# Kernel tuning notes

Hardware: AMD Instinct MI355X
Metric: run time of the kernel (lower is better)

## Reference

```python
import jax, jax.numpy as jnp
import numpy as np

B, N, D, H, HD, C = 2, 2048, 2048, 16, 128, 128  # batch, seq, embed, heads, head_dim, chunk
EPS = 1e-6


def setup_inputs() -> dict:
    key = jax.random.key(0)
    ks = jax.random.split(key, 9)
    s = 0.02
    x = jax.random.normal(ks[0], (B, N, D), jnp.float32)
    # per-head negative log decay (lambda = exp(log_decay) in (0,1))
    log_decay = -jax.random.uniform(ks[1], (H,), jnp.float32, minval=0.01, maxval=1.0)
    Wq = jax.random.normal(ks[2], (D, D), jnp.float32) * s
    Wk = jax.random.normal(ks[3], (D, D), jnp.float32) * s
    Wv = jax.random.normal(ks[4], (D, D), jnp.float32) * s
    Wo = jax.random.normal(ks[5], (D, D), jnp.float32) * s
    Wg1 = jax.random.normal(ks[6], (D, HD), jnp.float32) * s
    Wg2 = jax.random.normal(ks[7], (HD, D), jnp.float32) * s
    norm_w = jnp.ones((D,), jnp.float32)
    return dict(x=x, log_decay=log_decay, Wq=Wq, Wk=Wk, Wv=Wv, Wo=Wo,
                Wg1=Wg1, Wg2=Wg2, norm_w=norm_w)


def _lasd(q, k, v, ld):
    # causal linear attention with per-head scalar log-decay, chunked scan.
    # q,k,v: [B,N,H,HD]; ld: [H] (negative). Recurrence: S_t = exp(ld)*S_{t-1} + k_t v_t^T; o_t = q_t @ S_t
    nc = N // C
    to_chunks = lambda t: t.reshape(B, nc, C, H, HD).transpose(1, 0, 3, 2, 4)  # [nc,B,H,C,HD]
    qc, kc, vc = map(to_chunks, (q, k, v))
    i = jnp.arange(C, dtype=jnp.float32)
    diff = i[:, None] - i[None, :]                     # [C,C]
    Dm = jnp.exp(jnp.where(diff >= 0, ld[:, None, None] * diff, -jnp.inf))  # [H,C,C]
    dq = jnp.exp(ld[:, None] * (i + 1.0))              # [H,C] decay applied to q vs chunk-start state
    dk = jnp.exp(ld[:, None] * (C - 1.0 - i))          # [H,C] decay applied to k for state update
    dS = jnp.exp(ld * C)                               # [H]   chunk-level state decay

    def step(S, qkv):
        qb, kb, vb = qkv                               # [B,H,C,HD]
        attn = jnp.einsum('bhid,bhjd->bhij', qb, kb) * Dm
        o = jnp.einsum('bhij,bhje->bhie', attn, vb)
        o = o + jnp.einsum('bhid,bhde->bhie', qb * dq[None, :, :, None], S)
        S = S * dS[None, :, None, None] + jnp.einsum('bhjd,bhje->bhde', kb * dk[None, :, :, None], vb)
        return S, o

    S0 = jnp.zeros((B, H, HD, HD), jnp.float32)
    _, o = jax.lax.scan(step, S0, (qc, kc, vc))        # [nc,B,H,C,HD]
    return o.transpose(1, 0, 3, 2, 4).reshape(B, N, H, HD)


def reference(x, log_decay, Wq, Wk, Wv, Wo, Wg1, Wg2, norm_w):
    silu = jax.nn.silu
    q = silu(x @ Wq).reshape(B, N, H, HD)
    k = silu(x @ Wk).reshape(B, N, H, HD)
    v = silu(x @ Wv).reshape(B, N, H, HD)
    o = _lasd(q, k, v, log_decay).reshape(B, N, D)
    gate = jax.nn.sigmoid((x @ Wg1) @ Wg2)             # two stacked linears, no nonlinearity between
    o = o * gate
    o = o * jax.lax.rsqrt(jnp.mean(o * o, axis=-1, keepdims=True) + EPS) * norm_w  # rmsnorm
    return o @ Wo
```

## Files before the change

### kernel.cpp

```cpp
#include <hip/hip_runtime.h>
#include <hip/hip_bf16.h>
#include <cstdint>
#include <cstddef>

#define B_   2
#define N_   2048
#define D_   2048
#define H_   16
#define HD_  128
#define C_   128
#define NC_  16
#define M_   4096
#define QKVG_ 8192

typedef __attribute__((ext_vector_type(8))) short bf16x8;
typedef __attribute__((ext_vector_type(4))) float f32x4;
typedef __attribute__((ext_vector_type(16))) float f32x16;

__device__ __forceinline__ uint16_t f2bf(float f){
  __hip_bfloat16 h = __float2bfloat16(f);
  return *reinterpret_cast<uint16_t*>(&h);
}
__device__ __forceinline__ float bf2f(uint16_t u){
  union { uint32_t i; float f; } v; v.i = ((uint32_t)u) << 16; return v.f;
}

__device__ __forceinline__ void async16(const uint16_t* g, uint16_t* l){
  __builtin_amdgcn_global_load_lds(
      (const __attribute__((address_space(1))) void*)g,
      (__attribute__((address_space(3))) void*)l, 16, 0, 0);
}

__device__ __forceinline__ int swz(int row, int c){
  return row*128 + ((((c >> 3) ^ row) & 15) << 3) + (c & 7);
}

__global__ __launch_bounds__(256) void cast_kernel(
    const float* __restrict__ x, uint16_t* __restrict__ y)
{
  int i = (blockIdx.x*256 + threadIdx.x)*4;
  float4 f = *(const float4*)(x + i);
  ushort4 u;
  u.x = f2bf(f.x); u.y = f2bf(f.y); u.z = f2bf(f.z); u.w = f2bf(f.w);
  *(ushort4*)(y + i) = u;
}

__global__ __launch_bounds__(256)
void prep_weights(const float* __restrict__ Wq, const float* __restrict__ Wk,
                  const float* __restrict__ Wv, const float* __restrict__ Wo,
                  const float* __restrict__ Wg2, const float* __restrict__ Wg1,
                  uint16_t* __restrict__ WT, uint16_t* __restrict__ WoT,
                  uint16_t* __restrict__ Wg2T, uint16_t* __restrict__ Wg1b)
{
  const int z = blockIdx.z;
  const int tx = threadIdx.x & 31;
  const int ty = threadIdx.x >> 5;
  __shared__ uint16_t tile[32][33];

  if (z == 5){
    if (blockIdx.x >= 4) return;
    const int r0 = blockIdx.y*32, c0 = blockIdx.x*32;
    #pragma unroll
    for (int rr = 0; rr < 4; ++rr){
      int r = r0 + ty + rr*8;
      Wg1b[(size_t)r*HD_ + c0 + tx] = f2bf(Wg1[(size_t)r*HD_ + c0 + tx]);
    }
    return;
  }

  const float* src; uint16_t* dst; int R, Cc;
  if (z < 3)      { src = (z==0)?Wq:(z==1)?Wk:Wv; dst = WT + (size_t)z*D_*D_; R = D_; Cc = D_; }
  else if (z == 3){ src = Wo;  dst = WoT;  R = D_;  Cc = D_; }
  else            { if (blockIdx.y >= 4) return;
                    src = Wg2; dst = Wg2T; R = HD_; Cc = D_; }

  const int r0 = blockIdx.y*32, c0 = blockIdx.x*32;
  #pragma unroll
  for (int rr = 0; rr < 4; ++rr){
    int r = ty + rr*8;
    tile[r][tx] = f2bf(src[(size_t)(r0 + r)*Cc + c0 + tx]);
  }
  __syncthreads();
  #pragma unroll
  for (int rr = 0; rr < 4; ++rr){
    int r = ty + rr*8;
    dst[(size_t)(c0 + r)*R + r0 + tx] = tile[tx][r];
  }
}

template<int ACT, int OUTBF>
__global__ __launch_bounds__(256)
void gemm_bt2(const uint16_t* __restrict__ A, const uint16_t* __restrict__ Bt,
              void* __restrict__ Cout, int M, int Ncols, int K, int klen)
{
  __shared__ __align__(16) uint16_t As[128*64];
  __shared__ __align__(16) uint16_t Bs[128*64];
  const int t    = threadIdx.x;
  const int lane = t & 63, wave = t >> 6;
  const int wm = wave >> 1, wn = wave & 1;
  const int row0 = wm*64, col0 = wn*64;
  const int lm = lane & 31, lh = lane >> 5;

  const uint16_t* Ap = A  + (size_t)(blockIdx.y*128)*K;
  const uint16_t* Bp = Bt + (size_t)(blockIdx.x*128)*K;
  const int kbeg = blockIdx.z * klen;

  f32x16 acc[2][2];
  #pragma unroll
  for (int i = 0; i < 2; ++i)
    #pragma unroll
    for (int j = 0; j < 2; ++j)
      #pragma unroll
      for (int r = 0; r < 16; ++r) acc[i][j][r] = 0.f;

  const int srow = t >> 3;
  const int gch  = (t & 7) ^ (srow & 7);
  const size_t aoff0 = (size_t)srow*K + gch*8;

  for (int k0 = kbeg; k0 < kbeg + klen; k0 += 64){
    #pragma unroll
    for (int c = 0; c < 4; ++c){
      async16(Ap + (size_t)(c*32)*K + aoff0 + k0, As + c*2048 + t*8);
      async16(Bp + (size_t)(c*32)*K + aoff0 + k0, Bs + c*2048 + t*8);
    }
    __syncthreads();
    #pragma unroll
    for (int kh = 0; kh < 4; ++kh){
      bf16x8 af[2], bfr[2];
      const int ch = kh*2 + lh;
      #pragma unroll
      for (int i = 0; i < 2; ++i){
        int r = row0 + i*32 + lm;
        af[i] = *(const bf16x8*)(As + r*64 + ((ch ^ (r & 7)) << 3));
      }
      #pragma unroll
      for (int j = 0; j < 2; ++j){
        int r = col0 + j*32 + lm;
        bfr[j] = *(const bf16x8*)(Bs + r*64 + ((ch ^ (r & 7)) << 3));
      }
      #pragma unroll
      for (int i = 0; i < 2; ++i)
        #pragma unroll
        for (int j = 0; j < 2; ++j)
          acc[i][j] = __builtin_amdgcn_mfma_f32_32x32x16_bf16(af[i], bfr[j], acc[i][j], 0, 0, 0);
    }
    __syncthreads();
  }

  const int mode = (ACT == 3) ? ((blockIdx.x < 48) ? 1 : 2) : ACT;
  uint16_t* outb = (uint16_t*)Cout;
  float*    outf = (float*)Cout + (OUTBF ? 0 : (size_t)blockIdx.z*M*Ncols);
  #pragma unroll
  for (int i = 0; i < 2; ++i){
    #pragma unroll
    for (int j = 0; j < 2; ++j){
      #pragma unroll
      for (int r = 0; r < 16; ++r){
        int row = blockIdx.y*128 + row0 + i*32 + (r & 3) + 8*(r >> 2) + 4*lh;
        int col = blockIdx.x*128 + col0 + j*32 + lm;
        float v = acc[i][j][r];
        if (mode == 1)      v = v / (1.f + __expf(-v));
        else if (mode == 2) v = 1.f / (1.f + __expf(-v));
        size_t off = (size_t)row*Ncols + col;
        if (OUTBF) outb[off] = f2bf(v);
        else       outf[off] = v;
      }
    }
  }
}

__global__ __launch_bounds__(256)
void add_kernel(const float* __restrict__ p0, const float* __restrict__ p1,
                float* __restrict__ out)
{
  int i = (blockIdx.x*256 + threadIdx.x)*4;
  float4 a = *(const float4*)(p0 + i);
  float4 b = *(const float4*)(p1 + i);
  float4 o; o.x = a.x+b.x; o.y = a.y+b.y; o.z = a.z+b.z; o.w = a.w+b.w;
  *(float4*)(out + i) = o;
}

__global__ __launch_bounds__(256)
void chunk_state_kernel(const uint16_t* __restrict__ qkvg,
                        const float* __restrict__ log_decay, uint16_t* __restrict__ MsumT)
{
  __shared__ __align__(16) uint16_t vT[128*128];
  __shared__ __align__(16) uint16_t kT[128*128];
  const int h = blockIdx.x, b = blockIdx.y, ic = blockIdx.z;
  const int t    = threadIdx.x;
  const int lane = t & 63, wave = t >> 6;
  const int wm = wave >> 1, wn = wave & 1;
  const int e0 = wm*64, d0 = wn*64;
  const int lr = lane & 15, kq = lane >> 4;
  const float ld = log_decay[h];
  const size_t rowbase = (size_t)b*N_ + (size_t)ic*C_;
  const uint16_t* kb = qkvg + (size_t)D_;
  const uint16_t* vb = qkvg + (size_t)2*D_;

  #pragma unroll 4
  for (int it = 0; it < 64; ++it){
    int idx = t + it*256;
    int j = idx >> 7, e = idx & 127;
    uint16_t vv = vb[(rowbase + j)*QKVG_ + h*HD_ + e];
    float kf = bf2f(kb[(rowbase + j)*QKVG_ + h*HD_ + e]) * __expf(ld * (float)(C_ - 1 - j));
    vT[swz(e, j)] = vv;
    kT[swz(e, j)] = f2bf(kf);
  }
  __syncthreads();

  const f32x4 zero = {0.f, 0.f, 0.f, 0.f};
  f32x4 acc[4][4];
  #pragma unroll
  for (int i = 0; i < 4; ++i)
    #pragma unroll
    for (int j = 0; j < 4; ++j) acc[i][j] = zero;

  #pragma unroll
  for (int kt = 0; kt < 4; ++kt){
    bf16x8 af[4], bfr[4];
    #pragma unroll
    for (int i = 0; i < 4; ++i)
      af[i]  = *(const bf16x8*)(vT + swz(e0 + i*16 + lr, kt*32 + kq*8));
    #pragma unroll
    for (int j = 0; j < 4; ++j)
      bfr[j] = *(const bf16x8*)(kT + swz(d0 + j*16 + lr, kt*32 + kq*8));
    #pragma unroll
    for (int i = 0; i < 4; ++i)
      #pragma unroll
      for (int j = 0; j < 4; ++j)
        acc[i][j] = __builtin_amdgcn_mfma_f32_16x16x32_bf16(af[i], bfr[j], acc[i][j], 0, 0, 0);
  }

  uint16_t* Mout = MsumT + (((size_t)ic*B_ + b)*H_ + h)*(size_t)(HD_*HD_);
  #pragma unroll
  for (int i = 0; i < 4; ++i)
    #pragma unroll
    for (int j = 0; j < 4; ++j)
      #pragma unroll
      for (int r = 0; r < 4; ++r)
        Mout[(size_t)(e0 + i*16 + kq*4 + r)*HD_ + d0 + j*16 + lr] = f2bf(acc[i][j][r]);
}

__global__ __launch_bounds__(256)
void scan_kernel(const uint16_t* __restrict__ MsumT, const float* __restrict__ log_decay,
                 uint16_t* __restrict__ StT)
{
  const int h = blockIdx.x, b = blockIdx.y;
  const float ld = log_decay[h];
  const float dS = __expf(ld * (float)C_);
  const int base_e = blockIdx.z*2048;
  float cur[8];
  #pragma unroll
  for (int r = 0; r < 8; ++r) cur[r] = 0.f;
  for (int i = 0; i < NC_; ++i){
    const size_t base = (((size_t)i*B_ + b)*H_ + h)*(size_t)(HD_*HD_) + base_e;
    #pragma unroll
    for (int r = 0; r < 8; ++r){
      int idx = threadIdx.x + r*256;
      StT[base + idx] = f2bf(cur[r]);
      cur[r] = cur[r]*dS + bf2f(MsumT[base + idx]);
    }
  }
}

__global__ __launch_bounds__(256)
void attn_kernel(const uint16_t* __restrict__ qkvg, const uint16_t* __restrict__ StT,
                 const float* __restrict__ log_decay, float* __restrict__ o_attn)
{
  __shared__ __align__(16) uint16_t Ps[128*128];
  __shared__ __align__(16) uint16_t vT[128*128];
  const int h = blockIdx.x, b = blockIdx.y, ic = blockIdx.z;
  const int t    = threadIdx.x;
  const int lane = t & 63, wave = t >> 6;
  const int wm = wave >> 1, wn = wave & 1;
  const int row0 = wm*64, col0 = wn*64;
  const int lr = lane & 15, kq = lane >> 4;
  const float ld = log_decay[h];
  const size_t rowbase = (size_t)b*N_ + (size_t)ic*C_;
  const uint16_t* qb = qkvg;
  const uint16_t* kb = qkvg + (size_t)D_;
  const uint16_t* vb = qkvg + (size_t)2*D_;

  #pragma unroll 4
  for (int it = 0; it < 64; ++it){
    int idx = t + it*256;
    int j = idx >> 7, e = idx & 127;
    vT[swz(e, j)] = vb[(rowbase + j)*QKVG_ + h*HD_ + e];
  }

  const f32x4 zero = {0.f, 0.f, 0.f, 0.f};
  f32x4 acc[4][4];
  #pragma unroll
  for (int i = 0; i < 4; ++i)
    #pragma unroll
    for (int j = 0; j < 4; ++j) acc[i][j] = zero;

  #pragma unroll
  for (int kt = 0; kt < 4; ++kt){
    bf16x8 af[4], bfr[4];
    #pragma unroll
    for (int i = 0; i < 4; ++i)
      af[i]  = *(const bf16x8*)(qb + (rowbase + row0 + i*16 + lr)*QKVG_ + h*HD_ + kt*32 + kq*8);
    #pragma unroll
    for (int j = 0; j < 4; ++j)
      bfr[j] = *(const bf16x8*)(kb + (rowbase + col0 + j*16 + lr)*QKVG_ + h*HD_ + kt*32 + kq*8);
    #pragma unroll
    for (int i = 0; i < 4; ++i)
      #pragma unroll
      for (int j = 0; j < 4; ++j)
        acc[i][j] = __builtin_amdgcn_mfma_f32_16x16x32_bf16(af[i], bfr[j], acc[i][j], 0, 0, 0);
  }
  #pragma unroll
  for (int i = 0; i < 4; ++i)
    #pragma unroll
    for (int j = 0; j < 4; ++j)
      #pragma unroll
      for (int r = 0; r < 4; ++r){
        int row = row0 + i*16 + kq*4 + r;
        int col = col0 + j*16 + lr;
        int dlt = row - col;
        float f = (dlt >= 0) ? __expf(ld * (float)dlt) : 0.f;
        Ps[swz(row, col)] = f2bf(acc[i][j][r] * f);
      }

  #pragma unroll
  for (int i = 0; i < 4; ++i)
    #pragma unroll
    for (int j = 0; j < 4; ++j) acc[i][j] = zero;
  const uint16_t* Sb = StT + (((size_t)ic*B_ + b)*H_ + h)*(size_t)(HD_*HD_);
  #pragma unroll
  for (int kt = 0; kt < 4; ++kt){
    bf16x8 af[4], bfr[4];
    #pragma unroll
    for (int i = 0; i < 4; ++i)
      af[i]  = *(const bf16x8*)(qb + (rowbase + row0 + i*16 + lr)*QKVG_ + h*HD_ + kt*32 + kq*8);
    #pragma unroll
    for (int j = 0; j < 4; ++j)
      bfr[j] = *(const bf16x8*)(Sb + (size_t)(col0 + j*16 + lr)*HD_ + kt*32 + kq*8);
    #pragma unroll
    for (int i = 0; i < 4; ++i)
      #pragma unroll
      for (int j = 0; j < 4; ++j)
        acc[i][j] = __builtin_amdgcn_mfma_f32_16x16x32_bf16(af[i], bfr[j], acc[i][j], 0, 0, 0);
  }
  #pragma unroll
  for (int i = 0; i < 4; ++i)
    #pragma unroll
    for (int r = 0; r < 4; ++r){
      float dqv = __expf(ld * (float)(row0 + i*16 + kq*4 + r + 1));
      #pragma unroll
      for (int j = 0; j < 4; ++j) acc[i][j][r] *= dqv;
    }

  __syncthreads();

  #pragma unroll
  for (int kt = 0; kt < 4; ++kt){
    bf16x8 af[4], bfr[4];
    #pragma unroll
    for (int i = 0; i < 4; ++i)
      af[i]  = *(const bf16x8*)(Ps + swz(row0 + i*16 + lr, kt*32 + kq*8));
    #pragma unroll
    for (int j = 0; j < 4; ++j)
      bfr[j] = *(const bf16x8*)(vT + swz(col0 + j*16 + lr, kt*32 + kq*8));
    #pragma unroll
    for (int i = 0; i < 4; ++i)
      #pragma unroll
      for (int j = 0; j < 4; ++j)
        acc[i][j] = __builtin_amdgcn_mfma_f32_16x16x32_bf16(af[i], bfr[j], acc[i][j], 0, 0, 0);
  }

  #pragma unroll
  for (int i = 0; i < 4; ++i)
    #pragma unroll
    for (int j = 0; j < 4; ++j)
      #pragma unroll
      for (int r = 0; r < 4; ++r){
        int row = row0 + i*16 + kq*4 + r;
        int col = col0 + j*16 + lr;
        o_attn[(rowbase + row)*D_ + h*HD_ + col] = acc[i][j][r];
      }
}

__global__ __launch_bounds__(256)
void gate_norm_kernel(const float* __restrict__ o_attn, const uint16_t* __restrict__ qkvg,
                      const float* __restrict__ norm_w, uint16_t* __restrict__ on)
{
  const int row = blockIdx.x;
  const int t = threadIdx.x;
  const int c1 = t*4, c2 = 1024 + t*4;
  const float*    orow = o_attn + (size_t)row*D_;
  const uint16_t* grow = qkvg + (size_t)row*QKVG_ + 3*D_;
  float4  o1 = *(const float4*)(orow + c1);
  float4  o2 = *(const float4*)(orow + c2);
  ushort4 g1 = *(const ushort4*)(grow + c1);
  ushort4 g2 = *(const ushort4*)(grow + c2);
  float v[8];
  v[0] = o1.x*bf2f(g1.x); v[1] = o1.y*bf2f(g1.y); v[2] = o1.z*bf2f(g1.z); v[3] = o1.w*bf2f(g1.w);
  v[4] = o2.x*bf2f(g2.x); v[5] = o2.y*bf2f(g2.y); v[6] = o2.z*bf2f(g2.z); v[7] = o2.w*bf2f(g2.w);
  float s = 0.f;
  #pragma unroll
  for (int k = 0; k < 8; ++k) s += v[k]*v[k];
  #pragma unroll
  for (int off = 32; off > 0; off >>= 1) s += __shfl_down(s, off);
  __shared__ float red[4];
  if ((t & 63) == 0) red[t >> 6] = s;
  __syncthreads();
  float total = red[0] + red[1] + red[2] + red[3];
  float scale = rsqrtf(total * (1.f/(float)D_) + 1e-6f);
  float4 w1 = *(const float4*)(norm_w + c1);
  float4 w2 = *(const float4*)(norm_w + c2);
  ushort4 b1, b2;
  b1.x = f2bf(v[0]*scale*w1.x); b1.y = f2bf(v[1]*scale*w1.y);
  b1.z = f2bf(v[2]*scale*w1.z); b1.w = f2bf(v[3]*scale*w1.w);
  b2.x = f2bf(v[4]*scale*w2.x); b2.y = f2bf(v[5]*scale*w2.y);
  b2.z = f2bf(v[6]*scale*w2.z); b2.w = f2bf(v[7]*scale*w2.w);
  *(ushort4*)(on + (size_t)row*D_ + c1) = b1;
  *(ushort4*)(on + (size_t)row*D_ + c2) = b2;
}

extern "C" void kernel_launch(void* const* d_in, const int* in_sizes, int n_in,
                              void* d_out, int out_size, void* d_ws, size_t ws_size,
                              hipStream_t stream) {
  const float* x         = (const float*)d_in[0];
  const float* log_decay = (const float*)d_in[1];
  const float* Wq        = (const float*)d_in[2];
  const float* Wk        = (const float*)d_in[3];
  const float* Wv        = (const float*)d_in[4];
  const float* Wo        = (const float*)d_in[5];
  const float* Wg1       = (const float*)d_in[6];
  const float* Wg2       = (const float*)d_in[7];
  const float* norm_w    = (const float*)d_in[8];
  float* out = (float*)d_out;

  uint8_t* p = (uint8_t*)d_ws;
  uint16_t* xb    = (uint16_t*)p; p += (size_t)M_*D_*2;
  uint16_t* WT    = (uint16_t*)p; p += (size_t)QKVG_*D_*2;
  uint16_t* WoT   = (uint16_t*)p; p += (size_t)D_*D_*2;
  uint16_t* Wg1b  = (uint16_t*)p; p += (size_t)D_*HD_*2;
  uint16_t* Wg2T  = (uint16_t*)p; p += (size_t)D_*HD_*2;
  uint16_t* qkvg  = (uint16_t*)p; p += (size_t)M_*QKVG_*2;
  uint16_t* MsumT = (uint16_t*)p; p += (size_t)NC_*B_*H_*HD_*HD_*2;
  uint16_t* StT   = (uint16_t*)p; p += (size_t)NC_*B_*H_*HD_*HD_*2;
  float*    o_att = (float*)WT;
  uint16_t* on    = xb;
  float*    part  = (float*)qkvg;

  cast_kernel<<<(M_*D_)/1024, 256, 0, stream>>>(x, xb);
  prep_weights<<<dim3(64, 64, 6), 256, 0, stream>>>(Wq, Wk, Wv, Wo, Wg2, Wg1,
                                                    WT, WoT, Wg2T, Wg1b);

  gemm_bt2<0,1><<<dim3(D_/128, D_/128, 1), 256, 0, stream>>>(
      Wg2T, Wg1b, WT + (size_t)3*D_*D_, D_, D_, HD_, HD_);

  gemm_bt2<3,1><<<dim3(QKVG_/128, M_/128, 1), 256, 0, stream>>>(
      xb, WT, qkvg, M_, QKVG_, D_, D_);

  chunk_state_kernel<<<dim3(H_, B_, NC_), 256, 0, stream>>>(qkvg, log_decay, MsumT);
  scan_kernel<<<dim3(H_, B_, 8), 256, 0, stream>>>(MsumT, log_decay, StT);
  attn_kernel<<<dim3(H_, B_, NC_), 256, 0, stream>>>(qkvg, StT, log_decay, o_att);

  gate_norm_kernel<<<M_, 256, 0, stream>>>(o_att, qkvg, norm_w, on);
  gemm_bt2<0,0><<<dim3(D_/128, M_/128, 2), 256, 0, stream>>>(
      on, WoT, part, M_, D_, D_, D_/2);
  add_kernel<<<(M_*D_)/1024, 256, 0, stream>>>(part, part + (size_t)M_*D_, out);
}
```

Measured before the change: 449.9 us.

## Emit transposed K/V tiles from QKVG GEMM epilogue and merge prep kernels

The QKVG projection now has its own GEMM kernel whose epilogue also writes per-chunk transposed V and decay-scaled transposed K tiles to global memory. The chunk-state and attention kernels read these directly instead of gathering and transposing through shared memory. The input cast is folded into the weight-prep launch, the attention kernel computes the QK^T and Q·S products in one pass, and the attention output is stored in bf16 instead of fp32. The cost is extra scattered, uncoalesced transposed writes in the GEMM epilogue and slightly lower precision on the attention output.

```diff
diff --git a/kernel.cpp b/kernel.cpp
--- a/kernel.cpp
+++ b/kernel.cpp
@@ -35,28 +35,29 @@
   return row*128 + ((((c >> 3) ^ row) & 15) << 3) + (c & 7);
 }
 
-__global__ __launch_bounds__(256) void cast_kernel(
-    const float* __restrict__ x, uint16_t* __restrict__ y)
-{
-  int i = (blockIdx.x*256 + threadIdx.x)*4;
-  float4 f = *(const float4*)(x + i);
-  ushort4 u;
-  u.x = f2bf(f.x); u.y = f2bf(f.y); u.z = f2bf(f.z); u.w = f2bf(f.w);
-  *(ushort4*)(y + i) = u;
-}
-
-__global__ __launch_bounds__(256)
-void prep_weights(const float* __restrict__ Wq, const float* __restrict__ Wk,
-                  const float* __restrict__ Wv, const float* __restrict__ Wo,
-                  const float* __restrict__ Wg2, const float* __restrict__ Wg1,
-                  uint16_t* __restrict__ WT, uint16_t* __restrict__ WoT,
-                  uint16_t* __restrict__ Wg2T, uint16_t* __restrict__ Wg1b)
+__global__ __launch_bounds__(256)
+void prep_all(const float* __restrict__ Wq, const float* __restrict__ Wk,
+              const float* __restrict__ Wv, const float* __restrict__ Wo,
+              const float* __restrict__ Wg2, const float* __restrict__ Wg1,
+              const float* __restrict__ x,
+              uint16_t* __restrict__ WT, uint16_t* __restrict__ WoT,
+              uint16_t* __restrict__ Wg2T, uint16_t* __restrict__ Wg1b,
+              uint16_t* __restrict__ xb)
 {
   const int z = blockIdx.z;
   const int tx = threadIdx.x & 31;
   const int ty = threadIdx.x >> 5;
   __shared__ uint16_t tile[32][33];
 
+  if (z >= 6){
+    const int r0 = (z-6)*2048 + blockIdx.y*32, c0 = blockIdx.x*32;
+    #pragma unroll
+    for (int rr = 0; rr < 4; ++rr){
+      int r = r0 + ty + rr*8;
+      xb[(size_t)r*D_ + c0 + tx] = f2bf(x[(size_t)r*D_ + c0 + tx]);
+    }
+    return;
+  }
   if (z == 5){
     if (blockIdx.x >= 4) return;
     const int r0 = blockIdx.y*32, c0 = blockIdx.x*32;
@@ -147,7 +148,6 @@
     __syncthreads();
   }
 
-  const int mode = (ACT == 3) ? ((blockIdx.x < 48) ? 1 : 2) : ACT;
   uint16_t* outb = (uint16_t*)Cout;
   float*    outf = (float*)Cout + (OUTBF ? 0 : (size_t)blockIdx.z*M*Ncols);
   #pragma unroll
@@ -159,11 +159,102 @@
         int row = blockIdx.y*128 + row0 + i*32 + (r & 3) + 8*(r >> 2) + 4*lh;
         int col = blockIdx.x*128 + col0 + j*32 + lm;
         float v = acc[i][j][r];
-        if (mode == 1)      v = v / (1.f + __expf(-v));
-        else if (mode == 2) v = 1.f / (1.f + __expf(-v));
+        if (ACT == 1)      v = v / (1.f + __expf(-v));
+        else if (ACT == 2) v = 1.f / (1.f + __expf(-v));
         size_t off = (size_t)row*Ncols + col;
         if (OUTBF) outb[off] = f2bf(v);
         else       outf[off] = v;
+      }
+    }
+  }
+}
+
+__global__ __launch_bounds__(256)
+void gemm_qkvg(const uint16_t* __restrict__ A, const uint16_t* __restrict__ Bt,
+               uint16_t* __restrict__ qkvg, uint16_t* __restrict__ vTg,
+               uint16_t* __restrict__ kTs, const float* __restrict__ log_decay)
+{
+  const int K = D_;
+  __shared__ __align__(16) uint16_t As[128*64];
+  __shared__ __align__(16) uint16_t Bs[128*64];
+  const int t    = threadIdx.x;
+  const int lane = t & 63, wave = t >> 6;
+  const int wm = wave >> 1, wn = wave & 1;
+  const int row0 = wm*64, col0 = wn*64;
+  const int lm = lane & 31, lh = lane >> 5;
+
+  const uint16_t* Ap = A  + (size_t)(blockIdx.y*128)*K;
+  const uint16_t* Bp = Bt + (size_t)(blockIdx.x*128)*K;
+
+  f32x16 acc[2][2];
+  #pragma unroll
+  for (int i = 0; i < 2; ++i)
+    #pragma unroll
+    for (int j = 0; j < 2; ++j)
+      #pragma unroll
+      for (int r = 0; r < 16; ++r) acc[i][j][r] = 0.f;
+
+  const int srow = t >> 3;
+  const int gch  = (t & 7) ^ (srow & 7);
+  const size_t aoff0 = (size_t)srow*K + gch*8;
+
+  for (int k0 = 0; k0 < K; k0 += 64){
+    #pragma unroll
+    for (int c = 0; c < 4; ++c){
+      async16(Ap + (size_t)(c*32)*K + aoff0 + k0, As + c*2048 + t*8);
+      async16(Bp + (size_t)(c*32)*K + aoff0 + k0, Bs + c*2048 + t*8);
+    }
+    __syncthreads();
+    #pragma unroll
+    for (int kh = 0; kh < 4; ++kh){
+      bf16x8 af[2], bfr[2];
+      const int ch = kh*2 + lh;
+      #pragma unroll
+      for (int i = 0; i < 2; ++i){
+        int r = row0 + i*32 + lm;
+        af[i] = *(const bf16x8*)(As + r*64 + ((ch ^ (r & 7)) << 3));
+      }
+      #pragma unroll
+      for (int j = 0; j < 2; ++j){
+        int r = col0 + j*32 + lm;
+        bfr[j] = *(const bf16x8*)(Bs + r*64 + ((ch ^ (r & 7)) << 3));
+      }
+      #pragma unroll
+      for (int i = 0; i < 2; ++i)
+        #pragma unroll
+        for (int j = 0; j < 2; ++j)
+          acc[i][j] = __builtin_amdgcn_mfma_f32_32x32x16_bf16(af[i], bfr[j], acc[i][j], 0, 0, 0);
+    }
+    __syncthreads();
+  }
+
+  const int sec = blockIdx.x >> 4;
+  const int h   = blockIdx.x & 15;
+  const int bb  = blockIdx.y >> 4;
+  const int ic  = blockIdx.y & 15;
+  const float ld = log_decay[h];
+  uint16_t* tdst = (sec == 2 ? vTg : kTs) +
+                   (((size_t)bb*H_ + h)*NC_ + ic)*(size_t)(HD_*C_);
+  #pragma unroll
+  for (int i = 0; i < 2; ++i){
+    #pragma unroll
+    for (int j = 0; j < 2; ++j){
+      #pragma unroll
+      for (int r = 0; r < 16; ++r){
+        int rloc = row0 + i*32 + (r & 3) + 8*(r >> 2) + 4*lh;
+        int cloc = col0 + j*32 + lm;
+        float v = acc[i][j][r];
+        if (sec < 3) v = v / (1.f + __expf(-v));
+        else         v = 1.f / (1.f + __expf(-v));
+        if (sec == 2){
+          tdst[(size_t)cloc*C_ + rloc] = f2bf(v);
+        } else {
+          size_t row = (size_t)blockIdx.y*128 + rloc;
+          qkvg[row*QKVG_ + (size_t)blockIdx.x*128 + cloc] = f2bf(v);
+          if (sec == 1)
+            tdst[(size_t)cloc*C_ + rloc] =
+                f2bf(v * __expf(ld * (float)(C_ - 1 - rloc)));
+        }
       }
     }
   }
@@ -181,32 +272,16 @@
 }
 
 __global__ __launch_bounds__(256)
-void chunk_state_kernel(const uint16_t* __restrict__ qkvg,
-                        const float* __restrict__ log_decay, uint16_t* __restrict__ MsumT)
-{
-  __shared__ __align__(16) uint16_t vT[128*128];
-  __shared__ __align__(16) uint16_t kT[128*128];
+void chunk_state_kernel(const uint16_t* __restrict__ vTg, const uint16_t* __restrict__ kTs,
+                        uint16_t* __restrict__ MsumT)
+{
   const int h = blockIdx.x, b = blockIdx.y, ic = blockIdx.z;
   const int t    = threadIdx.x;
   const int lane = t & 63, wave = t >> 6;
   const int wm = wave >> 1, wn = wave & 1;
   const int e0 = wm*64, d0 = wn*64;
   const int lr = lane & 15, kq = lane >> 4;
-  const float ld = log_decay[h];
-  const size_t rowbase = (size_t)b*N_ + (size_t)ic*C_;
-  const uint16_t* kb = qkvg + (size_t)D_;
-  const uint16_t* vb = qkvg + (size_t)2*D_;
-
-  #pragma unroll 4
-  for (int it = 0; it < 64; ++it){
-    int idx = t + it*256;
-    int j = idx >> 7, e = idx & 127;
-    uint16_t vv = vb[(rowbase + j)*QKVG_ + h*HD_ + e];
-    float kf = bf2f(kb[(rowbase + j)*QKVG_ + h*HD_ + e]) * __expf(ld * (float)(C_ - 1 - j));
-    vT[swz(e, j)] = vv;
-    kT[swz(e, j)] = f2bf(kf);
-  }
-  __syncthreads();
+  const size_t tbase = (((size_t)b*H_ + h)*NC_ + ic)*(size_t)(HD_*C_);
 
   const f32x4 zero = {0.f, 0.f, 0.f, 0.f};
   f32x4 acc[4][4];
@@ -220,10 +295,10 @@
     bf16x8 af[4], bfr[4];
     #pragma unroll
     for (int i = 0; i < 4; ++i)
-      af[i]  = *(const bf16x8*)(vT + swz(e0 + i*16 + lr, kt*32 + kq*8));
+      af[i]  = *(const bf16x8*)(vTg + tbase + (size_t)(e0 + i*16 + lr)*C_ + kt*32 + kq*8);
     #pragma unroll
     for (int j = 0; j < 4; ++j)
-      bfr[j] = *(const bf16x8*)(kT + swz(d0 + j*16 + lr, kt*32 + kq*8));
+      bfr[j] = *(const bf16x8*)(kTs + tbase + (size_t)(d0 + j*16 + lr)*C_ + kt*32 + kq*8);
     #pragma unroll
     for (int i = 0; i < 4; ++i)
       #pragma unroll
@@ -264,11 +339,11 @@
 }
 
 __global__ __launch_bounds__(256)
-void attn_kernel(const uint16_t* __restrict__ qkvg, const uint16_t* __restrict__ StT,
-                 const float* __restrict__ log_decay, float* __restrict__ o_attn)
+void attn_kernel(const uint16_t* __restrict__ qkvg, const uint16_t* __restrict__ vTg,
+                 const uint16_t* __restrict__ StT, const float* __restrict__ log_decay,
+                 uint16_t* __restrict__ o_attb)
 {
   __shared__ __align__(16) uint16_t Ps[128*128];
-  __shared__ __align__(16) uint16_t vT[128*128];
   const int h = blockIdx.x, b = blockIdx.y, ic = blockIdx.z;
   const int t    = threadIdx.x;
   const int lane = t & 63, wave = t >> 6;
@@ -279,37 +354,70 @@
   const size_t rowbase = (size_t)b*N_ + (size_t)ic*C_;
   const uint16_t* qb = qkvg;
   const uint16_t* kb = qkvg + (size_t)D_;
-  const uint16_t* vb = qkvg + (size_t)2*D_;
-
-  #pragma unroll 4
-  for (int it = 0; it < 64; ++it){
-    int idx = t + it*256;
-    int j = idx >> 7, e = idx & 127;
-    vT[swz(e, j)] = vb[(rowbase + j)*QKVG_ + h*HD_ + e];
-  }
+  const uint16_t* Sb = StT + (((size_t)ic*B_ + b)*H_ + h)*(size_t)(HD_*HD_);
+  const uint16_t* vb = vTg + (((size_t)b*H_ + h)*NC_ + ic)*(size_t)(HD_*C_);
 
   const f32x4 zero = {0.f, 0.f, 0.f, 0.f};
-  f32x4 acc[4][4];
+  f32x4 accP[4][4], accO[4][4];
   #pragma unroll
   for (int i = 0; i < 4; ++i)
     #pragma unroll
-    for (int j = 0; j < 4; ++j) acc[i][j] = zero;
+    for (int j = 0; j < 4; ++j){ accP[i][j] = zero; accO[i][j] = zero; }
 
   #pragma unroll
   for (int kt = 0; kt < 4; ++kt){
-    bf16x8 af[4], bfr[4];
+    bf16x8 af[4], bk[4], bS[4];
     #pragma unroll
     for (int i = 0; i < 4; ++i)
-      af[i]  = *(const bf16x8*)(qb + (rowbase + row0 + i*16 + lr)*QKVG_ + h*HD_ + kt*32 + kq*8);
+      af[i] = *(const bf16x8*)(qb + (rowbase + row0 + i*16 + lr)*QKVG_ + h*HD_ + kt*32 + kq*8);
+    #pragma unroll
+    for (int j = 0; j < 4; ++j){
+      bk[j] = *(const bf16x8*)(kb + (rowbase + col0 + j*16 + lr)*QKVG_ + h*HD_ + kt*32 + kq*8);
+      bS[j] = *(const bf16x8*)(Sb + (size_t)(col0 + j*16 + lr)*HD_ + kt*32 + kq*8);
+    }
+    #pragma unroll
+    for (int i = 0; i < 4; ++i)
+      #pragma unroll
+      for (int j = 0; j < 4; ++j){
+        accP[i][j] = __builtin_amdgcn_mfma_f32_16x16x32_bf16(af[i], bk[j], accP[i][j], 0, 0, 0);
+        accO[i][j] = __builtin_amdgcn_mfma_f32_16x16x32_bf16(af[i], bS[j], accO[i][j], 0, 0, 0);
+      }
+  }
+
+  #pragma unroll
+  for (int i = 0; i < 4; ++i)
+    #pragma unroll
+    for (int r = 0; r < 4; ++r){
+      int row = row0 + i*16 + kq*4 + r;
+      float dqv = __expf(ld * (float)(row + 1));
+      #pragma unroll
+      for (int j = 0; j < 4; ++j){
+        int col = col0 + j*16 + lr;
+        int dlt = row - col;
+        float f = (dlt >= 0) ? __expf(ld * (float)dlt) : 0.f;
+        Ps[swz(row, col)] = f2bf(accP[i][j][r] * f);
+        accO[i][j][r] *= dqv;
+      }
+    }
+
+  __syncthreads();
+
+  #pragma unroll
+  for (int kt = 0; kt < 4; ++kt){
+    bf16x8 af[4], bv[4];
+    #pragma unroll
+    for (int i = 0; i < 4; ++i)
+      af[i] = *(const bf16x8*)(Ps + swz(row0 + i*16 + lr, kt*32 + kq*8));
     #pragma unroll
     for (int j = 0; j < 4; ++j)
-      bfr[j] = *(const bf16x8*)(kb + (rowbase + col0 + j*16 + lr)*QKVG_ + h*HD_ + kt*32 + kq*8);
+      bv[j] = *(const bf16x8*)(vb + (size_t)(col0 + j*16 + lr)*C_ + kt*32 + kq*8);
     #pragma unroll
     for (int i = 0; i < 4; ++i)
       #pragma unroll
       for (int j = 0; j < 4; ++j)
-        acc[i][j] = __builtin_amdgcn_mfma_f32_16x16x32_bf16(af[i], bfr[j], acc[i][j], 0, 0, 0);
-  }
+        accO[i][j] = __builtin_amdgcn_mfma_f32_16x16x32_bf16(af[i], bv[j], accO[i][j], 0, 0, 0);
+  }
+
   #pragma unroll
   for (int i = 0; i < 4; ++i)
     #pragma unroll
@@ -318,86 +426,28 @@
       for (int r = 0; r < 4; ++r){
         int row = row0 + i*16 + kq*4 + r;
         int col = col0 + j*16 + lr;
-        int dlt = row - col;
-        float f = (dlt >= 0) ? __expf(ld * (float)dlt) : 0.f;
-        Ps[swz(row, col)] = f2bf(acc[i][j][r] * f);
-      }
-
-  #pragma unroll
-  for (int i = 0; i < 4; ++i)
-    #pragma unroll
-    for (int j = 0; j < 4; ++j) acc[i][j] = zero;
-  const uint16_t* Sb = StT + (((size_t)ic*B_ + b)*H_ + h)*(size_t)(HD_*HD_);
-  #pragma unroll
-  for (int kt = 0; kt < 4; ++kt){
-    bf16x8 af[4], bfr[4];
-    #pragma unroll
-    for (int i = 0; i < 4; ++i)
-      af[i]  = *(const bf16x8*)(qb + (rowbase + row0 + i*16 + lr)*QKVG_ + h*HD_ + kt*32 + kq*8);
-    #pragma unroll
-    for (int j = 0; j < 4; ++j)
-      bfr[j] = *(const bf16x8*)(Sb + (size_t)(col0 + j*16 + lr)*HD_ + kt*32 + kq*8);
-    #pragma unroll
-    for (int i = 0; i < 4; ++i)
-      #pragma unroll
-      for (int j = 0; j < 4; ++j)
-        acc[i][j] = __builtin_amdgcn_mfma_f32_16x16x32_bf16(af[i], bfr[j], acc[i][j], 0, 0, 0);
-  }
-  #pragma unroll
-  for (int i = 0; i < 4; ++i)
-    #pragma unroll
-    for (int r = 0; r < 4; ++r){
-      float dqv = __expf(ld * (float)(row0 + i*16 + kq*4 + r + 1));
-      #pragma unroll
-      for (int j = 0; j < 4; ++j) acc[i][j][r] *= dqv;
-    }
-
-  __syncthreads();
-
-  #pragma unroll
-  for (int kt = 0; kt < 4; ++kt){
-    bf16x8 af[4], bfr[4];
-    #pragma unroll
-    for (int i = 0; i < 4; ++i)
-      af[i]  = *(const bf16x8*)(Ps + swz(row0 + i*16 + lr, kt*32 + kq*8));
-    #pragma unroll
-    for (int j = 0; j < 4; ++j)
-      bfr[j] = *(const bf16x8*)(vT + swz(col0 + j*16 + lr, kt*32 + kq*8));
-    #pragma unroll
-    for (int i = 0; i < 4; ++i)
-      #pragma unroll
-      for (int j = 0; j < 4; ++j)
-        acc[i][j] = __builtin_amdgcn_mfma_f32_16x16x32_bf16(af[i], bfr[j], acc[i][j], 0, 0, 0);
-  }
-
-  #pragma unroll
-  for (int i = 0; i < 4; ++i)
-    #pragma unroll
-    for (int j = 0; j < 4; ++j)
-      #pragma unroll
-      for (int r = 0; r < 4; ++r){
-        int row = row0 + i*16 + kq*4 + r;
-        int col = col0 + j*16 + lr;
-        o_attn[(rowbase + row)*D_ + h*HD_ + col] = acc[i][j][r];
-      }
-}
-
-__global__ __launch_bounds__(256)
-void gate_norm_kernel(const float* __restrict__ o_attn, const uint16_t* __restrict__ qkvg,
+        o_attb[(rowbase + row)*D_ + h*HD_ + col] = f2bf(accO[i][j][r]);
+      }
+}
+
+__global__ __launch_bounds__(256)
+void gate_norm_kernel(const uint16_t* __restrict__ o_attb, const uint16_t* __restrict__ qkvg,
                       const float* __restrict__ norm_w, uint16_t* __restrict__ on)
 {
   const int row = blockIdx.x;
   const int t = threadIdx.x;
   const int c1 = t*4, c2 = 1024 + t*4;
-  const float*    orow = o_attn + (size_t)row*D_;
+  const uint16_t* orow = o_attb + (size_t)row*D_;
   const uint16_t* grow = qkvg + (size_t)row*QKVG_ + 3*D_;
-  float4  o1 = *(const float4*)(orow + c1);
-  float4  o2 = *(const float4*)(orow + c2);
+  ushort4 o1 = *(const ushort4*)(orow + c1);
+  ushort4 o2 = *(const ushort4*)(orow + c2);
   ushort4 g1 = *(const ushort4*)(grow + c1);
   ushort4 g2 = *(const ushort4*)(grow + c2);
   float v[8];
-  v[0] = o1.x*bf2f(g1.x); v[1] = o1.y*bf2f(g1.y); v[2] = o1.z*bf2f(g1.z); v[3] = o1.w*bf2f(g1.w);
-  v[4] = o2.x*bf2f(g2.x); v[5] = o2.y*bf2f(g2.y); v[6] = o2.z*bf2f(g2.z); v[7] = o2.w*bf2f(g2.w);
+  v[0] = bf2f(o1.x)*bf2f(g1.x); v[1] = bf2f(o1.y)*bf2f(g1.y);
+  v[2] = bf2f(o1.z)*bf2f(g1.z); v[3] = bf2f(o1.w)*bf2f(g1.w);
+  v[4] = bf2f(o2.x)*bf2f(g2.x); v[5] = bf2f(o2.y)*bf2f(g2.y);
+  v[6] = bf2f(o2.z)*bf2f(g2.z); v[7] = bf2f(o2.w)*bf2f(g2.w);
   float s = 0.f;
   #pragma unroll
   for (int k = 0; k < 8; ++k) s += v[k]*v[k];
@@ -440,27 +490,28 @@
   uint16_t* Wg1b  = (uint16_t*)p; p += (size_t)D_*HD_*2;
   uint16_t* Wg2T  = (uint16_t*)p; p += (size_t)D_*HD_*2;
   uint16_t* qkvg  = (uint16_t*)p; p += (size_t)M_*QKVG_*2;
+  uint16_t* vTg   = (uint16_t*)p; p += (size_t)B_*H_*NC_*HD_*C_*2;
+  uint16_t* kTs   = (uint16_t*)p; p += (size_t)B_*H_*NC_*HD_*C_*2;
   uint16_t* MsumT = (uint16_t*)p; p += (size_t)NC_*B_*H_*HD_*HD_*2;
   uint16_t* StT   = (uint16_t*)p; p += (size_t)NC_*B_*H_*HD_*HD_*2;
-  float*    o_att = (float*)WT;
+  uint16_t* o_attb= WT;
   uint16_t* on    = xb;
   float*    part  = (float*)qkvg;
 
-  cast_kernel<<<(M_*D_)/1024, 256, 0, stream>>>(x, xb);
-  prep_weights<<<dim3(64, 64, 6), 256, 0, stream>>>(Wq, Wk, Wv, Wo, Wg2, Wg1,
-                                                    WT, WoT, Wg2T, Wg1b);
+  prep_all<<<dim3(64, 64, 8), 256, 0, stream>>>(Wq, Wk, Wv, Wo, Wg2, Wg1, x,
+                                                WT, WoT, Wg2T, Wg1b, xb);
 
   gemm_bt2<0,1><<<dim3(D_/128, D_/128, 1), 256, 0, stream>>>(
       Wg2T, Wg1b, WT + (size_t)3*D_*D_, D_, D_, HD_, HD_);
 
-  gemm_bt2<3,1><<<dim3(QKVG_/128, M_/128, 1), 256, 0, stream>>>(
-      xb, WT, qkvg, M_, QKVG_, D_, D_);
-
-  chunk_state_kernel<<<dim3(H_, B_, NC_), 256, 0, stream>>>(qkvg, log_decay, MsumT);
+  gemm_qkvg<<<dim3(QKVG_/128, M_/128, 1), 256, 0, stream>>>(
+      xb, WT, qkvg, vTg, kTs, log_decay);
+
+  chunk_state_kernel<<<dim3(H_, B_, NC_), 256, 0, stream>>>(vTg, kTs, MsumT);
   scan_kernel<<<dim3(H_, B_, 8), 256, 0, stream>>>(MsumT, log_decay, StT);
-  attn_kernel<<<dim3(H_, B_, NC_), 256, 0, stream>>>(qkvg, StT, log_decay, o_att);
-
-  gate_norm_kernel<<<M_, 256, 0, stream>>>(o_att, qkvg, norm_w, on);
+  attn_kernel<<<dim3(H_, B_, NC_), 256, 0, stream>>>(qkvg, vTg, StT, log_decay, o_attb);
+
+  gate_norm_kernel<<<M_, 256, 0, stream>>>(o_attb, qkvg, norm_w, on);
   gemm_bt2<0,0><<<dim3(D_/128, M_/128, 2), 256, 0, stream>>>(
       on, WoT, part, M_, D_, D_, D_/2);
   add_kernel<<<(M_*D_)/1024, 256, 0, stream>>>(part, part + (size_t)M_*D_, out);
```

Result: slower. 469.5 us (+4.4%).
